# Kernel tuning notes

Hardware: AMD Instinct MI355X
Metric: run time of the kernel (lower is better)

The kernel has to match this reference:

```python
import jax, jax.numpy as jnp
import numpy as np

DECAY = 0.9      # LIF membrane decay per step
V_TH = 1.0       # spike threshold


def setup_inputs() -> dict:
    key = jax.random.key(0)
    k1, k2, k3, k4, k5 = jax.random.split(key, 5)
    B, D, N = 256, 1024, 2048
    density = 0.3
    external_inputs = jax.random.normal(k1, (B, D), dtype=jnp.float32)
    # nn.Linear(input_dim, num_neurons): weight [N, D], bias [N]
    W_in = jax.random.normal(k2, (N, D), dtype=jnp.float32) / np.sqrt(D)
    b_in = jnp.zeros((N,), dtype=jnp.float32)
    adj_weights = jax.random.normal(k3, (N, N), dtype=jnp.float32) * 0.01
    mask = (jax.random.uniform(k4, (N, N)) < density).astype(jnp.float32)
    mask = mask * (1.0 - jnp.eye(N, dtype=jnp.float32))  # zero diagonal
    return {
        "external_inputs": external_inputs,
        "W_in": W_in,
        "b_in": b_in,
        "adj_weights": adj_weights,
        "mask": mask,
        "time_steps": 64,
    }


def _spike(x):
    # Heaviside spike: 1 if membrane exceeds threshold
    return (x >= 0.0).astype(x.dtype)


def reference(external_inputs, W_in, b_in, adj_weights, mask, time_steps):
    B = external_inputs.shape[0]
    N = adj_weights.shape[0]
    I_ext = external_inputs @ W_in.T + b_in              # [B, N]
    W_eff = adj_weights * mask                           # [N, N]
    V0 = jnp.zeros((B, N), dtype=external_inputs.dtype)
    s0 = jnp.zeros((B, N), dtype=external_inputs.dtype)

    def step(carry, _):
        V, s = carry
        I_total = I_ext + s @ W_eff.T                    # recurrent current
        V = DECAY * V + I_total                          # LIF integration
        s_new = _spike(V - V_TH)
        V = V * (1.0 - s_new)                            # reset on spike
        return (V, s_new), s_new

    (_, _), spike_hist = jax.lax.scan(step, (V0, s0), None, length=time_steps)
    return spike_hist.mean(axis=0)                       # [B, N] firing rates
```

## Files before the change

### kernel.cpp

```cpp
#include <hip/hip_runtime.h>
#include <cstdint>
#include <cstddef>

#define N_NEU 2048
#define D_IN  1024
#define T_STEPS 64

typedef _Float16 f16x8 __attribute__((ext_vector_type(8)));
typedef _Float16 f16x4 __attribute__((ext_vector_type(4)));
typedef float    f32x4 __attribute__((ext_vector_type(4)));
typedef unsigned u32x4 __attribute__((ext_vector_type(4)));

#define MFMA16(a, b, c) __builtin_amdgcn_mfma_f32_16x16x32_f16((a), (b), (c), 0, 0, 0)


__device__ inline f16x8 expand8(unsigned b) {
  u32x4 t;
  t[0] = ((b & 1u)   ? 0x3C00u : 0u) | ((b & 2u)   ? 0x3C000000u : 0u);
  t[1] = ((b & 4u)   ? 0x3C00u : 0u) | ((b & 8u)   ? 0x3C000000u : 0u);
  t[2] = ((b & 16u)  ? 0x3C00u : 0u) | ((b & 32u)  ? 0x3C000000u : 0u);
  t[3] = ((b & 64u)  ? 0x3C00u : 0u) | ((b & 128u) ? 0x3C000000u : 0u);
  return __builtin_bit_cast(f16x8, t);
}

__global__ __launch_bounds__(256) void k_wsplit(const float* __restrict__ adj,
                                                const float* __restrict__ mask,
                                                _Float16* __restrict__ Wh,
                                                _Float16* __restrict__ Wl,
                                                unsigned long long* __restrict__ bmv) {
  const int idx = blockIdx.x * 256 + threadIdx.x;
  if (idx < 2 * 256 * 64) bmv[idx] = 0ull;
  const int total4 = (N_NEU * N_NEU) / 4;
  for (int i = idx; i < total4; i += gridDim.x * 256) {
    float4 a = ((const float4*)adj)[i];
    float4 m = ((const float4*)mask)[i];
    float w0 = a.x * m.x, w1 = a.y * m.y, w2 = a.z * m.z, w3 = a.w * m.w;
    f16x4 h, lo;
    h[0] = (_Float16)w0; lo[0] = (_Float16)((w0 - (float)h[0]) * 4096.0f);
    h[1] = (_Float16)w1; lo[1] = (_Float16)((w1 - (float)h[1]) * 4096.0f);
    h[2] = (_Float16)w2; lo[2] = (_Float16)((w2 - (float)h[2]) * 4096.0f);
    h[3] = (_Float16)w3; lo[3] = (_Float16)((w3 - (float)h[3]) * 4096.0f);
    ((f16x4*)Wh)[i] = h;
    ((f16x4*)Wl)[i] = lo;
  }
}

__global__ __launch_bounds__(256) void k_iext(const float* __restrict__ ext,
                                              const float* __restrict__ Win,
                                              const float* __restrict__ bin,
                                              float* __restrict__ Iext) {
  __shared__ float At[32][68];
  __shared__ float Bt[32][68];
  const int tid = threadIdx.x;
  const int b0 = (blockIdx.x & 3) * 64;
  const int n0 = (blockIdx.x >> 2) * 64;
  const int tx = tid & 15, ty = tid >> 4;
  float acc[4][4] = {};
  for (int kt = 0; kt < D_IN / 32; ++kt) {
    const int k0 = kt * 32;
#pragma unroll
    for (int i = 0; i < 8; ++i) {
      int e = tid + i * 256;
      int kk = e & 31, row = e >> 5;
      At[kk][row] = ext[(size_t)(b0 + row) * D_IN + k0 + kk];
      Bt[kk][row] = Win[(size_t)(n0 + row) * D_IN + k0 + kk];
    }
    __syncthreads();
    for (int kk = 0; kk < 32; ++kk) {
      f32x4 a = *(const f32x4*)&At[kk][ty * 4];
      f32x4 b = *(const f32x4*)&Bt[kk][tx * 4];
#pragma unroll
      for (int i = 0; i < 4; ++i)
#pragma unroll
        for (int j = 0; j < 4; ++j) acc[i][j] += a[i] * b[j];
    }
    __syncthreads();
  }
#pragma unroll
  for (int i = 0; i < 4; ++i)
#pragma unroll
    for (int j = 0; j < 4; ++j)
      Iext[(size_t)(b0 + ty * 4 + i) * N_NEU + n0 + tx * 4 + j] = acc[i][j] + bin[n0 + tx * 4 + j];
}

__global__ __launch_bounds__(512, 2) void k_fused8(
    const _Float16* __restrict__ Wh, const _Float16* __restrict__ Wl,
    const float* __restrict__ Iext, unsigned long long* __restrict__ bmv,
    float* __restrict__ out) {
  __shared__ float red[4 * 32 * 32];
  __shared__ unsigned bmA[32 * 64];
  __shared__ unsigned bmB[32 * 64];

  const int tid = threadIdx.x;
  const int lane = tid & 63;
  const int kw = tid >> 6;
  const int l15 = lane & 15;
  const int klo = lane >> 4;
  const int sh = klo * 8;
  const int gp = blockIdx.x >> 6;
  const int ns = blockIdx.x & 63;
  const int n0 = ns * 32;
  const int gA = gp, gB = gp + 4;
  const float inv4096 = 1.0f / 4096.0f;
  const f32x4 z4 = {0.f, 0.f, 0.f, 0.f};

  float IxA[2], IxB[2];
#pragma unroll
  for (int j = 0; j < 2; ++j) {
    IxA[j] = Iext[(size_t)(gA * 32 + j * 16 + (tid >> 5)) * N_NEU + n0 + (tid & 31)];
    IxB[j] = Iext[(size_t)(gB * 32 + j * 16 + (tid >> 5)) * N_NEU + n0 + (tid & 31)];
  }

  const _Float16* whb = Wh + (size_t)(n0 + l15) * N_NEU + kw * 256 + klo * 8;
  const _Float16* wlb = Wl + (size_t)(n0 + l15) * N_NEU + kw * 256 + klo * 8;
  f16x8 whf[2][8], wlf[2][8];
#pragma unroll
  for (int nt = 0; nt < 2; ++nt)
#pragma unroll
    for (int kcl = 0; kcl < 8; ++kcl) {
      whf[nt][kcl] = *(const f16x8*)(whb + nt * 16 * N_NEU + kcl * 32);
      wlf[nt][kcl] = *(const f16x8*)(wlb + nt * 16 * N_NEU + kcl * 32);
    }

  float VA[2] = {0.f, 0.f}, VB[2] = {0.f, 0.f};
  unsigned cA[2] = {0u, 0u}, cB[2] = {0u, 0u};
  unsigned long long vA[4], vB[4];

  auto spec_issue = [&](int g, int buf, unsigned long long (&v)[4]) {
    const unsigned long long* src = bmv + (size_t)buf * 16384 + (size_t)g * 2048 + tid;
#pragma unroll
    for (int i = 0; i < 4; ++i)
      v[i] = __hip_atomic_load(src + (size_t)i * 512, __ATOMIC_RELAXED, __HIP_MEMORY_SCOPE_AGENT);
  };
  auto check_retry = [&](int g, int buf, unsigned want, unsigned long long (&v)[4]) {
    const unsigned long long* src = bmv + (size_t)buf * 16384 + (size_t)g * 2048 + tid;
    unsigned need = 0u;
#pragma unroll
    for (int i = 0; i < 4; ++i)
      if ((unsigned)(v[i] >> 32) != want) need |= 1u << i;
    while (need) {
      __builtin_amdgcn_s_sleep(2);
#pragma unroll
      for (int i = 0; i < 4; ++i)
        if (need & (1u << i)) {
          v[i] = __hip_atomic_load(src + (size_t)i * 512,
                                   __ATOMIC_RELAXED, __HIP_MEMORY_SCOPE_AGENT);
          if ((unsigned)(v[i] >> 32) == want) need &= ~(1u << i);
        }
    }
  };
  auto stage = [&](unsigned* bm, const unsigned long long (&v)[4]) {
#pragma unroll
    for (int i = 0; i < 4; ++i) {
      const int w = i * 512 + tid, r = w >> 6, nsw = w & 63;
      bm[r * 64 + (nsw ^ ((r & 15) << 2))] = (unsigned)v[i];
    }
  };
  auto gemm = [&](const unsigned* bm, float (&cI)[2]) {
    f32x4 acch[2][2], accl[2][2];
#pragma unroll
    for (int mt = 0; mt < 2; ++mt)
#pragma unroll
      for (int nt = 0; nt < 2; ++nt) { acch[mt][nt] = z4; accl[mt][nt] = z4; }
#pragma unroll
    for (int mt = 0; mt < 2; ++mt) {
      const int row = mt * 16 + l15;
      const int swz = l15 << 2;
      const u32x4 q0 = *(const u32x4*)&bm[row * 64 + ((kw * 8) ^ swz)];
      const u32x4 q1 = *(const u32x4*)&bm[row * 64 + (((kw * 8) | 4) ^ swz)];
#pragma unroll
      for (int kcl = 0; kcl < 8; ++kcl) {
        const unsigned word = (kcl < 4) ? q0[kcl] : q1[kcl - 4];
        const f16x8 a = expand8((word >> sh) & 0xFFu);
        acch[mt][0] = MFMA16(a, whf[0][kcl], acch[mt][0]);
        accl[mt][0] = MFMA16(a, wlf[0][kcl], accl[mt][0]);
        acch[mt][1] = MFMA16(a, whf[1][kcl], acch[mt][1]);
        accl[mt][1] = MFMA16(a, wlf[1][kcl], accl[mt][1]);
      }
    }
    f32x4 cb[2][2];
#pragma unroll
    for (int mt = 0; mt < 2; ++mt)
#pragma unroll
      for (int nt = 0; nt < 2; ++nt) cb[mt][nt] = acch[mt][nt] + accl[mt][nt] * inv4096;
    const int cbn = lane & 15, rq = (lane >> 4) << 2;
    if (kw >= 4) {
      const int p = kw - 4;
#pragma unroll
      for (int mt = 0; mt < 2; ++mt)
#pragma unroll
        for (int nt = 0; nt < 2; ++nt) {
          const int col = nt * 16 + cbn;
          const int r0 = (mt * 16 + rq) ^ ((col & 7) << 2);
          *(f32x4*)(red + (p * 32 + col) * 32 + r0) = cb[mt][nt];
        }
    }
    __syncthreads();
    if (kw < 4) {
#pragma unroll
      for (int mt = 0; mt < 2; ++mt)
#pragma unroll
        for (int nt = 0; nt < 2; ++nt) {
          const int col = nt * 16 + cbn;
          const int r0 = (mt * 16 + rq) ^ ((col & 7) << 2);
          float* p2 = red + (kw * 32 + col) * 32 + r0;
          f32x4 o = *(const f32x4*)p2;
          o += cb[mt][nt];
          *(f32x4*)p2 = o;
        }
    }
    __syncthreads();
#pragma unroll
    for (int j = 0; j < 2; ++j) {
      const int o = j * 512 + tid;
      const int row = o >> 5, col = o & 31;
      const int rs = row ^ ((col & 7) << 2);
      float s = 0.0f;
#pragma unroll
      for (int p = 0; p < 4; ++p) s += red[(p * 32 + col) * 32 + rs];
      cI[j] = s;
    }
  };
  auto lif = [&](const float (&cI)[2], const float (&Ix)[2], float (&V)[2],
                 unsigned (&cnt)[2], int g, int nbuf, unsigned tag, bool dostore) {
#pragma unroll
    for (int j = 0; j < 2; ++j) {
      float I = cI[j] + Ix[j];
      float v = 0.9f * V[j] + I;
      bool sp = (v - 1.0f) >= 0.0f;
      V[j] = sp ? 0.0f : v;
      cnt[j] += sp ? 1u : 0u;
      if (dostore) {
        unsigned long long ba = __ballot(sp);
        const int rowf = g * 32 + j * 16 + kw * 2;
        const unsigned long long tg = ((unsigned long long)tag) << 32;
        if (lane == 0)
          __hip_atomic_store(bmv + (size_t)nbuf * 16384 + (size_t)rowf * 64 + ns,
                             tg | (unsigned)ba, __ATOMIC_RELAXED, __HIP_MEMORY_SCOPE_AGENT);
        else if (lane == 32)
          __hip_atomic_store(bmv + (size_t)nbuf * 16384 + (size_t)(rowf + 1) * 64 + ns,
                             tg | (unsigned)(ba >> 32), __ATOMIC_RELAXED, __HIP_MEMORY_SCOPE_AGENT);
      }
    }
  };

  {
    const float cz[2] = {0.f, 0.f};
    lif(cz, IxA, VA, cA, gA, 1, 1u, true);
    lif(cz, IxB, VB, cB, gB, 1, 1u, true);
    spec_issue(gA, 1, vA);
  }

  for (int t = 1; t < T_STEPS; ++t) {
    const int cbuf = t & 1, nbuf = (t + 1) & 1;
    const bool last = (t == T_STEPS - 1);
    float cI[2];

    check_retry(gA, cbuf, (unsigned)t, vA);
    stage(bmA, vA);
    __syncthreads();
    spec_issue(gB, cbuf, vB);
    gemm(bmA, cI);
    lif(cI, IxA, VA, cA, gA, nbuf, (unsigned)(t + 1), !last);

    check_retry(gB, cbuf, (unsigned)t, vB);
    stage(bmB, vB);
    __syncthreads();
    if (!last) spec_issue(gA, nbuf, vA);
    gemm(bmB, cI);
    lif(cI, IxB, VB, cB, gB, nbuf, (unsigned)(t + 1), !last);
  }

#pragma unroll
  for (int j = 0; j < 2; ++j) {
    const int rA = gA * 32 + j * 16 + (tid >> 5);
    const int rB = gB * 32 + j * 16 + (tid >> 5);
    out[(size_t)rA * N_NEU + n0 + (tid & 31)] = (float)cA[j] * 0.015625f;
    out[(size_t)rB * N_NEU + n0 + (tid & 31)] = (float)cB[j] * 0.015625f;
  }
}

extern "C" void kernel_launch(void* const* d_in, const int* in_sizes, int n_in,
                              void* d_out, int out_size, void* d_ws, size_t ws_size,
                              hipStream_t stream) {
  (void)in_sizes; (void)n_in; (void)out_size; (void)ws_size;
  const float* ext  = (const float*)d_in[0];
  const float* Win  = (const float*)d_in[1];
  const float* bin  = (const float*)d_in[2];
  const float* adj  = (const float*)d_in[3];
  const float* mask = (const float*)d_in[4];
  unsigned char* ws = (unsigned char*)d_ws;

  _Float16* Wh   = (_Float16*)(ws);
  _Float16* Wl   = (_Float16*)(ws + (size_t)(8u << 20));
  float*    Iext = (float*)   (ws + (size_t)(16u << 20));
  unsigned long long* bmv = (unsigned long long*)(ws + (size_t)(18u << 20));
  float* out = (float*)d_out;

  hipLaunchKernelGGL(k_wsplit, dim3(2048), dim3(256), 0, stream, adj, mask, Wh, Wl, bmv);
  hipLaunchKernelGGL(k_iext,   dim3(128),  dim3(256), 0, stream, ext, Win, bin, Iext);
  hipLaunchKernelGGL(k_fused8, dim3(256),  dim3(512), 0, stream,
                     Wh, Wl, Iext, bmv, out);
}
```

Measured before the change: 443.9 us.

## Use LUT bit expansion, single-barrier reduction, earlier speculative loads, shorter sleep

Replaces the per-bit select expansion of spike bitmasks with a 16-entry shared-memory lookup table producing two 64-bit halves. It widens the cross-wave reduction buffer so all eight waves write partials at once, removing one barrier and the read-modify-write pass in each step. It issues the speculative load of the second group's spike bitmap before polling the first, and shortens the spin sleep. The trade-offs are more LDS use and extra LDS lookups inside the MFMA loop, plus an earlier load that is more likely to see a stale tag and need retrying.

```diff
diff --git a/kernel.cpp b/kernel.cpp
--- a/kernel.cpp
+++ b/kernel.cpp
@@ -10,18 +10,10 @@
 typedef _Float16 f16x4 __attribute__((ext_vector_type(4)));
 typedef float    f32x4 __attribute__((ext_vector_type(4)));
 typedef unsigned u32x4 __attribute__((ext_vector_type(4)));
+typedef unsigned long long u64x2 __attribute__((ext_vector_type(2)));
 
 #define MFMA16(a, b, c) __builtin_amdgcn_mfma_f32_16x16x32_f16((a), (b), (c), 0, 0, 0)
 
-
-__device__ inline f16x8 expand8(unsigned b) {
-  u32x4 t;
-  t[0] = ((b & 1u)   ? 0x3C00u : 0u) | ((b & 2u)   ? 0x3C000000u : 0u);
-  t[1] = ((b & 4u)   ? 0x3C00u : 0u) | ((b & 8u)   ? 0x3C000000u : 0u);
-  t[2] = ((b & 16u)  ? 0x3C00u : 0u) | ((b & 32u)  ? 0x3C000000u : 0u);
-  t[3] = ((b & 64u)  ? 0x3C00u : 0u) | ((b & 128u) ? 0x3C000000u : 0u);
-  return __builtin_bit_cast(f16x8, t);
-}
 
 __global__ __launch_bounds__(256) void k_wsplit(const float* __restrict__ adj,
                                                 const float* __restrict__ mask,
@@ -83,13 +75,14 @@
       Iext[(size_t)(b0 + ty * 4 + i) * N_NEU + n0 + tx * 4 + j] = acc[i][j] + bin[n0 + tx * 4 + j];
 }
 
-__global__ __launch_bounds__(512, 2) void k_fused8(
+__global__ __launch_bounds__(512, 2) void k_fused10(
     const _Float16* __restrict__ Wh, const _Float16* __restrict__ Wl,
     const float* __restrict__ Iext, unsigned long long* __restrict__ bmv,
     float* __restrict__ out) {
-  __shared__ float red[4 * 32 * 32];
+  __shared__ float red[8 * 32 * 32];
   __shared__ unsigned bmA[32 * 64];
   __shared__ unsigned bmB[32 * 64];
+  __shared__ unsigned long long lut16[16];
 
   const int tid = threadIdx.x;
   const int lane = tid & 63;
@@ -104,6 +97,15 @@
   const float inv4096 = 1.0f / 4096.0f;
   const f32x4 z4 = {0.f, 0.f, 0.f, 0.f};
 
+  if (tid < 16) {
+    unsigned long long e = 0ull;
+    if (tid & 1) e |= 0x3C00ull;
+    if (tid & 2) e |= 0x3C00ull << 16;
+    if (tid & 4) e |= 0x3C00ull << 32;
+    if (tid & 8) e |= 0x3C00ull << 48;
+    lut16[tid] = e;
+  }
+
   float IxA[2], IxB[2];
 #pragma unroll
   for (int j = 0; j < 2; ++j) {
@@ -139,7 +141,7 @@
     for (int i = 0; i < 4; ++i)
       if ((unsigned)(v[i] >> 32) != want) need |= 1u << i;
     while (need) {
-      __builtin_amdgcn_s_sleep(2);
+      __builtin_amdgcn_s_sleep(1);
 #pragma unroll
       for (int i = 0; i < 4; ++i)
         if (need & (1u << i)) {
@@ -156,6 +158,12 @@
       bm[r * 64 + (nsw ^ ((r & 15) << 2))] = (unsigned)v[i];
     }
   };
+  auto exp8 = [&](unsigned b) -> f16x8 {
+    u64x2 t;
+    t[0] = lut16[b & 15u];
+    t[1] = lut16[(b >> 4) & 15u];
+    return __builtin_bit_cast(f16x8, t);
+  };
   auto gemm = [&](const unsigned* bm, float (&cI)[2]) {
     f32x4 acch[2][2], accl[2][2];
 #pragma unroll
@@ -171,7 +179,7 @@
 #pragma unroll
       for (int kcl = 0; kcl < 8; ++kcl) {
         const unsigned word = (kcl < 4) ? q0[kcl] : q1[kcl - 4];
-        const f16x8 a = expand8((word >> sh) & 0xFFu);
+        const f16x8 a = exp8((word >> sh) & 0xFFu);
         acch[mt][0] = MFMA16(a, whf[0][kcl], acch[mt][0]);
         accl[mt][0] = MFMA16(a, wlf[0][kcl], accl[mt][0]);
         acch[mt][1] = MFMA16(a, whf[1][kcl], acch[mt][1]);
@@ -184,31 +192,14 @@
 #pragma unroll
       for (int nt = 0; nt < 2; ++nt) cb[mt][nt] = acch[mt][nt] + accl[mt][nt] * inv4096;
     const int cbn = lane & 15, rq = (lane >> 4) << 2;
-    if (kw >= 4) {
-      const int p = kw - 4;
-#pragma unroll
-      for (int mt = 0; mt < 2; ++mt)
-#pragma unroll
-        for (int nt = 0; nt < 2; ++nt) {
-          const int col = nt * 16 + cbn;
-          const int r0 = (mt * 16 + rq) ^ ((col & 7) << 2);
-          *(f32x4*)(red + (p * 32 + col) * 32 + r0) = cb[mt][nt];
-        }
-    }
-    __syncthreads();
-    if (kw < 4) {
-#pragma unroll
-      for (int mt = 0; mt < 2; ++mt)
-#pragma unroll
-        for (int nt = 0; nt < 2; ++nt) {
-          const int col = nt * 16 + cbn;
-          const int r0 = (mt * 16 + rq) ^ ((col & 7) << 2);
-          float* p2 = red + (kw * 32 + col) * 32 + r0;
-          f32x4 o = *(const f32x4*)p2;
-          o += cb[mt][nt];
-          *(f32x4*)p2 = o;
-        }
-    }
+#pragma unroll
+    for (int mt = 0; mt < 2; ++mt)
+#pragma unroll
+      for (int nt = 0; nt < 2; ++nt) {
+        const int col = nt * 16 + cbn;
+        const int r0 = (mt * 16 + rq) ^ ((col & 7) << 2);
+        *(f32x4*)(red + (kw * 32 + col) * 32 + r0) = cb[mt][nt];
+      }
     __syncthreads();
 #pragma unroll
     for (int j = 0; j < 2; ++j) {
@@ -217,7 +208,7 @@
       const int rs = row ^ ((col & 7) << 2);
       float s = 0.0f;
 #pragma unroll
-      for (int p = 0; p < 4; ++p) s += red[(p * 32 + col) * 32 + rs];
+      for (int p = 0; p < 8; ++p) s += red[(p * 32 + col) * 32 + rs];
       cI[j] = s;
     }
   };
@@ -256,10 +247,10 @@
     const bool last = (t == T_STEPS - 1);
     float cI[2];
 
+    spec_issue(gB, cbuf, vB);
     check_retry(gA, cbuf, (unsigned)t, vA);
     stage(bmA, vA);
     __syncthreads();
-    spec_issue(gB, cbuf, vB);
     gemm(bmA, cI);
     lif(cI, IxA, VA, cA, gA, nbuf, (unsigned)(t + 1), !last);
 
@@ -299,6 +290,6 @@
 
   hipLaunchKernelGGL(k_wsplit, dim3(2048), dim3(256), 0, stream, adj, mask, Wh, Wl, bmv);
   hipLaunchKernelGGL(k_iext,   dim3(128),  dim3(256), 0, stream, ext, Win, bin, Iext);
-  hipLaunchKernelGGL(k_fused8, dim3(256),  dim3(512), 0, stream,
+  hipLaunchKernelGGL(k_fused10, dim3(256), dim3(512), 0, stream,
                      Wh, Wl, Iext, bmv, out);
 }
```

Measured after the change: 615.6 us. 38.7% more time.
